# Kernel optimization log

Hardware: AMD Instinct MI355X
Metric: run time of the kernel (lower is better)

The kernel has to match this reference:

```python
import jax, jax.numpy as jnp
import numpy as np

B, S, DIN, H, DOUT, E, SEL = 8, 2048, 512, 512, 512, 262144, 512
N = B * S


def setup_inputs() -> dict:
    key = jax.random.key(0)
    ks = jax.random.split(key, 20)
    inp = {
        "x": jax.random.normal(ks[0], (B, S, DIN), dtype=jnp.float32),
        "edge_index": jax.random.randint(ks[1], (2, E), 0, N, dtype=jnp.int64),
        "selected_idx": jax.random.randint(ks[2], (B, SEL), 0, S, dtype=jnp.int64),
        "edge_label": jax.random.randint(ks[3], (E,), 0, 8, dtype=jnp.int64),
    }
    k = 4
    for l, fin in enumerate([DIN, H, H]):
        inp[f"conv{l}_w1"] = jax.random.normal(ks[k], (2 * fin, H), dtype=jnp.float32) * 0.02; k += 1
        inp[f"conv{l}_b1"] = jnp.full((H,), 0.01, dtype=jnp.float32)
        inp[f"conv{l}_w2"] = jax.random.normal(ks[k], (H, H), dtype=jnp.float32) * 0.02; k += 1
        inp[f"conv{l}_b2"] = jnp.full((H,), 0.01, dtype=jnp.float32)
    inp["ffn_w1"] = jax.random.normal(ks[k], (H, H), dtype=jnp.float32) * 0.02; k += 1
    inp["ffn_b1"] = jnp.full((H,), 0.01, dtype=jnp.float32)
    inp["ffn_w2"] = jax.random.normal(ks[k], (H, DOUT), dtype=jnp.float32) * 0.02; k += 1
    inp["ffn_b2"] = jnp.full((DOUT,), 0.01, dtype=jnp.float32)
    return inp


def _ffw(x, w1, b1, w2, b2):
    # FeedForward: fc2(act_dropout(relu(fc1(x)))), dropout=0 in eval
    return jax.nn.relu(x @ w1 + b1) @ w2 + b2


def reference(x, edge_index, selected_idx, edge_label,
              conv0_w1, conv0_b1, conv0_w2, conv0_b2,
              conv1_w1, conv1_b1, conv1_w2, conv1_b2,
              conv2_w1, conv2_b1, conv2_w2, conv2_b2,
              ffn_w1, ffn_b1, ffn_w2, ffn_b2):
    b, s, d = x.shape
    n = b * s
    h = x.reshape(n, d)
    src, dst = edge_index[0], edge_index[1]  # PyG: x_j = source, x_i = target
    convs = [(conv0_w1, conv0_b1, conv0_w2, conv0_b2),
             (conv1_w1, conv1_b1, conv1_w2, conv1_b2),
             (conv2_w1, conv2_b1, conv2_w2, conv2_b2)]
    for w1, b1, w2, b2 in convs:
        xi = h[dst]                                   # [E, F]
        xj = h[src]
        ef = jnp.concatenate([xi, xj - xi], axis=1)   # [E, 2F]
        m = _ffw(ef, w1, b1, w2, b2)                  # per-edge MLP [E, H]
        agg = jax.ops.segment_max(m, dst, num_segments=n)
        agg = jnp.where(jnp.isneginf(agg), 0.0, agg)  # empty segments -> 0 (PyG fill)
        h = jax.nn.relu(agg)                          # dropout p acts as identity in eval
    h = _ffw(h, ffn_w1, ffn_b1, ffn_w2, ffn_b2)
    out = h.reshape(b, s, -1)                         # [B, S, DOUT]
    idx = jnp.broadcast_to(selected_idx[:, :, None], (b, selected_idx.shape[1], out.shape[-1]))
    return jnp.take_along_axis(out, idx, axis=1)      # [B, SEL, DOUT]
```

## Files before the change

### kernel.cpp

```cpp
#include <hip/hip_runtime.h>
#include <hip/hip_bf16.h>


#define N_NODES 16384
#define EDGES   262144
#define HDIM    512
#define SEQ     2048

typedef __attribute__((ext_vector_type(8))) short short8;
typedef __attribute__((ext_vector_type(8))) _Float16 half8;
typedef __attribute__((ext_vector_type(2))) _Float16 half2v;
typedef __attribute__((ext_vector_type(4))) float f32x4;

__device__ __forceinline__ void gld16(const void* g, void* l) {
    __builtin_amdgcn_global_load_lds(
        (const __attribute__((address_space(1))) void*)g,
        (__attribute__((address_space(3))) void*)l, 16, 0, 0);
}
__device__ __forceinline__ unsigned short f2b(float f) {
    unsigned int x = __float_as_uint(f);
    return (unsigned short)((x + 0x7fffu + ((x >> 16) & 1u)) >> 16);
}
__device__ __forceinline__ unsigned short f2h(float f) {
    _Float16 h = (_Float16)f;
    return __builtin_bit_cast(unsigned short, h);
}
__device__ __forceinline__ unsigned int zpack_h(unsigned int u, unsigned int v) {
    half2v a = __builtin_bit_cast(half2v, u);
    half2v b = __builtin_bit_cast(half2v, v);
    half2v s = a + b;
    half2v z = {(_Float16)0.f, (_Float16)0.f};
    half2v r = __builtin_elementwise_max(s, z);
    return __builtin_bit_cast(unsigned int, r);
}
__device__ __forceinline__ short8 frag_ld(const short* S, int row, int q) {
    int p = q ^ ((row >> 1) & 3);
    return *(const short8*)(S + row * 32 + p * 8);
}
__device__ __forceinline__ void stage_tile(const short* G, int kc, short* S, int t) {
#pragma unroll
    for (int it = 0; it < 2; ++it) {
        int lin = it * 256 + t;
        int row = lin >> 2, p = lin & 3;
        int q = p ^ ((row >> 1) & 3);
        gld16(G + (size_t)row * HDIM + kc + q * 8, S + lin * 8);
    }
}
__device__ __forceinline__ void mfma_tile_bf16(const short* As, const short* Bs,
                                               int wm, int wn, int l, f32x4 acc[4][4]) {
    short8 a[4], b[4];
#pragma unroll
    for (int mt = 0; mt < 4; ++mt) a[mt] = frag_ld(As, wm + mt * 16 + (l & 15), l >> 4);
#pragma unroll
    for (int nt = 0; nt < 4; ++nt) b[nt] = frag_ld(Bs, wn + nt * 16 + (l & 15), l >> 4);
#pragma unroll
    for (int mt = 0; mt < 4; ++mt)
#pragma unroll
        for (int nt = 0; nt < 4; ++nt)
            acc[mt][nt] = __builtin_amdgcn_mfma_f32_16x16x32_bf16(a[mt], b[nt], acc[mt][nt], 0, 0, 0);
}
__device__ __forceinline__ half8 frag64(const short* S, int row, int q) {
    int p = q ^ ((row >> 1) & 7) ^ (row & 1);
    return *(const half8*)(S + row * 64 + p * 8);
}
__device__ __forceinline__ void stageB32(const short* __restrict__ Wt, int n0, int col0,
                                         short* buf, int t) {
#pragma unroll
    for (int it = 0; it < 4; ++it) {
        int lin = it * 256 + t;
        int row = lin >> 2, s = lin & 3;
        int q = s ^ ((row >> 1) & 3);
        gld16(Wt + (size_t)(n0 + row) * HDIM + col0 + q * 8, buf + lin * 8);
    }
}

__global__ __launch_bounds__(256) void hist_kernel(
    const int* __restrict__ dst, int* __restrict__ hist) {
    int idx = blockIdx.x * 256 + threadIdx.x;
    atomicAdd(&hist[dst[idx]], 1);
}
__global__ __launch_bounds__(256) void scan_kernel(
    const int* __restrict__ hist, int* __restrict__ cursor) {
    __shared__ int part[256];
    const int t = threadIdx.x, base = t * 64;
    int sum = 0;
    for (int i = 0; i < 64; ++i) sum += hist[base + i];
    part[t] = sum;
    __syncthreads();
    int run = 0;
    for (int i = 0; i < t; ++i) run += part[i];
    for (int i = 0; i < 64; ++i) {
        int h = hist[base + i];
        cursor[base + i] = run;
        run += h;
    }
}
__global__ __launch_bounds__(256) void scatter_kernel(
    const int* __restrict__ dst, const int* __restrict__ src,
    int* __restrict__ cursor, int* __restrict__ dstS, int* __restrict__ srcS) {
    int idx = blockIdx.x * 256 + threadIdx.x;
    int d = dst[idx];
    int p = atomicAdd(&cursor[d], 1);
    dstS[p] = d;
    srcS[p] = src[idx];
}

__global__ __launch_bounds__(256) void prep_weights_kernel(
    const float* __restrict__ w1, const float* __restrict__ w2,
    short* __restrict__ WdT, short* __restrict__ w1bT, short* __restrict__ W2T) {
    __shared__ float tile[32][33];
    const int which = blockIdx.z;
    const int k0 = blockIdx.x * 32, n0 = blockIdx.y * 32;
    const int tx = threadIdx.x, ty = threadIdx.y;
#pragma unroll
    for (int i = 0; i < 4; ++i) {
        int k = k0 + ty + i * 8, n = n0 + tx;
        float v;
        if (which == 0)      v = w1[k * 512 + n] - w1[(k + 512) * 512 + n];
        else if (which == 1) v = w1[(k + 512) * 512 + n];
        else                 v = w2[k * 512 + n];
        tile[ty + i * 8][tx] = v;
    }
    __syncthreads();
    short* out = which == 0 ? WdT : (which == 1 ? w1bT : W2T);
#pragma unroll
    for (int i = 0; i < 4; ++i) {
        int n = n0 + ty + i * 8, k = k0 + tx;
        float v = tile[tx][ty + i * 8];
        out[(size_t)n * 512 + k] = (short)(which == 2 ? f2h(v) : f2b(v));
    }
}
__global__ __launch_bounds__(256) void tr_kernel(
    const float* __restrict__ W1, const float* __restrict__ W2,
    short* __restrict__ T1, short* __restrict__ T2) {
    __shared__ float tile[32][33];
    const float* W = blockIdx.z ? W2 : W1;
    short* T = blockIdx.z ? T2 : T1;
    const int k0 = blockIdx.x * 32, n0 = blockIdx.y * 32;
    const int tx = threadIdx.x, ty = threadIdx.y;
#pragma unroll
    for (int i = 0; i < 4; ++i)
        tile[ty + i * 8][tx] = W[(k0 + ty + i * 8) * 512 + n0 + tx];
    __syncthreads();
#pragma unroll
    for (int i = 0; i < 4; ++i)
        T[(size_t)(n0 + ty + i * 8) * 512 + k0 + tx] = (short)f2b(tile[tx][ty + i * 8]);
}
__global__ __launch_bounds__(256) void cvt_bf16_kernel(
    const float* __restrict__ x, short* __restrict__ xb) {
    int idx = blockIdx.x * 256 + threadIdx.x;
    float4 v = ((const float4*)x)[idx];
    uint2 o;
    o.x = (unsigned int)f2b(v.x) | ((unsigned int)f2b(v.y) << 16);
    o.y = (unsigned int)f2b(v.z) | ((unsigned int)f2b(v.w) << 16);
    ((uint2*)xb)[idx] = o;
}

__global__ __launch_bounds__(256) void node_gemm_uv_kernel(
    const short* __restrict__ A, const short* __restrict__ WdT,
    const short* __restrict__ w1bT, const float* __restrict__ b1,
    short* __restrict__ U, short* __restrict__ V) {
    __shared__ short As[128 * 32];
    __shared__ short Bs[128 * 32];
    const int t = threadIdx.x;
    const int by = blockIdx.y;
    const short* Wt = (by < 4) ? WdT : w1bT;
    short* C = (by < 4) ? U : V;
    const float* bias = (by < 4) ? b1 : nullptr;
    const int m0 = blockIdx.x * 128, n0 = (by & 3) * 128;
    const int w = t >> 6, l = t & 63;
    const int wm = (w & 1) * 64, wn = (w >> 1) * 64;
    f32x4 acc[4][4] = {};
    for (int kc = 0; kc < HDIM; kc += 32) {
        stage_tile(A + (size_t)m0 * HDIM, kc, As, t);
        stage_tile(Wt + (size_t)n0 * HDIM, kc, Bs, t);
        __syncthreads();
        mfma_tile_bf16(As, Bs, wm, wn, l, acc);
        __syncthreads();
    }
#pragma unroll
    for (int mt = 0; mt < 4; ++mt) {
        int m = m0 + wm + mt * 16 + (l >> 4) * 4;
#pragma unroll
        for (int nt = 0; nt < 4; ++nt) {
            int n = n0 + wn + nt * 16 + (l & 15);
            float bv = bias ? bias[n] : 0.f;
#pragma unroll
            for (int r = 0; r < 4; ++r)
                C[(size_t)(m + r) * HDIM + n] = (short)f2h(acc[mt][nt][r] + bv);
        }
    }
}

__device__ __forceinline__ unsigned int fkey(float m) {
    unsigned int b = __float_as_uint(m);
    return ((int)b < 0) ? ~b : (b | 0x80000000u);
}
__device__ __forceinline__ void kflush(unsigned int* K, int d, int col, float m) {
    atomicMax(K + (((size_t)d) << 9) + col, fkey(m));
}
__global__ __launch_bounds__(256, 3) void edge_mfma_kernel(
    const short* __restrict__ U, const short* __restrict__ V,
    const short* __restrict__ Wt, const int* __restrict__ srcS,
    const int* __restrict__ dstS, unsigned int* __restrict__ K) {
    __shared__ short As[64 * 64];
    __shared__ short Bs[2][256 * 32];
    __shared__ int sdst[64], ssrc[64];
    const int t = threadIdx.x;
    const int L  = blockIdx.x;
    const int g  = (L >> 4) * 8 + (L & 7);
    const int nh = (L >> 3) & 1;
    const int e0 = g * 64, n0 = nh * 256;
    if (t < 64) { sdst[t] = dstS[e0 + t]; ssrc[t] = srcS[e0 + t]; }
    __syncthreads();
    const int w = t >> 6, l = t & 63;
    const int wnb = w * 64;
    const int lm = l & 15;
    const int arow = t >> 2, s0 = (t & 3) * 2;
    const int perm = ((arow >> 1) & 7) ^ (arow & 1);
    const int p0 = s0 ^ perm, p1 = (s0 + 1) ^ perm;
    const short* up = U + (((size_t)sdst[arow]) << 9) + s0 * 8;
    const short* vp = V + (((size_t)ssrc[arow]) << 9) + s0 * 8;
    unsigned int* As_u = (unsigned int*)As;
    f32x4 acc[4][4] = {};
    uint4 pu0, pu1, pv0, pv1, nu0, nu1, nv0, nv1;
    stageB32(Wt, n0, 0, Bs[0], t);
    pu0 = *(const uint4*)(up);
    pu1 = *(const uint4*)(up + 8);
    pv0 = *(const uint4*)(vp);
    pv1 = *(const uint4*)(vp + 8);
#pragma unroll
    for (int hh = 0; hh < 16; ++hh) {
        const int kc = (hh >> 1) * 64;
        if (hh < 15) {
            const int c1 = ((hh + 1) >> 1) * 64 + ((hh + 1) & 1) * 32;
            stageB32(Wt, n0, c1, Bs[(hh + 1) & 1], t);
        }
        if ((hh & 1) == 0) {
            if (hh < 14) {
                nu0 = *(const uint4*)(up + kc + 64);
                nu1 = *(const uint4*)(up + kc + 64 + 8);
                nv0 = *(const uint4*)(vp + kc + 64);
                nv1 = *(const uint4*)(vp + kc + 64 + 8);
            }
            uint4 z0, z1;
            z0.x = zpack_h(pu0.x, pv0.x); z0.y = zpack_h(pu0.y, pv0.y);
            z0.z = zpack_h(pu0.z, pv0.z); z0.w = zpack_h(pu0.w, pv0.w);
            z1.x = zpack_h(pu1.x, pv1.x); z1.y = zpack_h(pu1.y, pv1.y);
            z1.z = zpack_h(pu1.z, pv1.z); z1.w = zpack_h(pu1.w, pv1.w);
            *(uint4*)(As_u + arow * 32 + p0 * 4) = z0;
            *(uint4*)(As_u + arow * 32 + p1 * 4) = z1;
        }
        if (hh < 14)       asm volatile("s_waitcnt vmcnt(8) lgkmcnt(0)" ::: "memory");
        else if (hh == 14) asm volatile("s_waitcnt vmcnt(4) lgkmcnt(0)" ::: "memory");
        else               asm volatile("s_waitcnt vmcnt(0) lgkmcnt(0)" ::: "memory");
        __builtin_amdgcn_s_barrier();
        asm volatile("" ::: "memory");
        const short* Bb = Bs[hh & 1];
        const int hq = (hh & 1) * 4 + (l >> 4);
        __builtin_amdgcn_s_setprio(1);
        half8 b[4];
#pragma unroll
        for (int nt = 0; nt < 4; ++nt) {
            int row = wnb + nt * 16 + lm;
            int p = (l >> 4) ^ ((row >> 1) & 3);
            b[nt] = *(const half8*)(Bb + row * 32 + p * 8);
        }
#pragma unroll
        for (int mt = 0; mt < 4; ++mt) {
            half8 a = frag64(As, mt * 16 + lm, hq);
#pragma unroll
            for (int nt = 0; nt < 4; ++nt)
                acc[mt][nt] = __builtin_amdgcn_mfma_f32_16x16x32_f16(a, b[nt], acc[mt][nt], 0, 0, 0);
        }
        __builtin_amdgcn_s_setprio(0);
        if ((hh & 1) == 0 && hh < 14) { pu0 = nu0; pu1 = nu1; pv0 = nv0; pv1 = nv1; }
        asm volatile("" ::: "memory");
        __builtin_amdgcn_s_barrier();
    }
    const int dbase = sdst[0];
    const int drange = sdst[63] - dbase + 1;
    unsigned int* tile = (unsigned int*)Bs[1];
    if (drange <= 16) {
#pragma unroll
        for (int i = 0; i < 16; ++i) tile[i * 256 + t] = 0u;
        __syncthreads();
#pragma unroll
        for (int mt = 0; mt < 4; ++mt) {
            int base = mt * 16 + (l >> 4) * 4;
            int d0 = sdst[base], d1 = sdst[base + 1], d2 = sdst[base + 2], d3 = sdst[base + 3];
            int r0 = d0 - dbase, r1 = d1 - dbase, r2 = d2 - dbase, r3 = d3 - dbase;
#pragma unroll
            for (int nt = 0; nt < 4; ++nt) {
                int colb = wnb + nt * 16 + lm;
                f32x4 a = acc[mt][nt];
                float m = a[0];
                if (d1 == d0) m = fmaxf(m, a[1]);
                else { atomicMax(tile + r0 * 256 + colb, fkey(m)); m = a[1]; }
                if (d2 == d1) m = fmaxf(m, a[2]);
                else { atomicMax(tile + r1 * 256 + colb, fkey(m)); m = a[2]; }
                if (d3 == d2) m = fmaxf(m, a[3]);
                else { atomicMax(tile + r2 * 256 + colb, fkey(m)); m = a[3]; }
                atomicMax(tile + r3 * 256 + colb, fkey(m));
            }
        }
        __syncthreads();
#pragma unroll 4
        for (int r = 0; r < 16; ++r) {
            if (r < drange) {
                unsigned int kv = tile[r * 256 + t];
                if (kv) atomicMax(K + (((size_t)(dbase + r)) << 9) + n0 + t, kv);
            }
        }
    } else {
#pragma unroll
        for (int mt = 0; mt < 4; ++mt) {
            int base = mt * 16 + (l >> 4) * 4;
            int d0 = sdst[base], d1 = sdst[base + 1], d2 = sdst[base + 2], d3 = sdst[base + 3];
#pragma unroll
            for (int nt = 0; nt < 4; ++nt) {
                int col = n0 + wnb + nt * 16 + lm;
                f32x4 a = acc[mt][nt];
                float m = a[0];
                if (d1 == d0) m = fmaxf(m, a[1]); else { kflush(K, d0, col, m); m = a[1]; }
                if (d2 == d1) m = fmaxf(m, a[2]); else { kflush(K, d1, col, m); m = a[2]; }
                if (d3 == d2) m = fmaxf(m, a[3]); else { kflush(K, d2, col, m); m = a[3]; }
                kflush(K, d3, col, m);
            }
        }
    }
}

__global__ __launch_bounds__(256) void decode_kernel(
    unsigned int* __restrict__ K, const float* __restrict__ b2,
    short* __restrict__ hb) {
    int idx = blockIdx.x * 256 + threadIdx.x;
    unsigned int k = K[idx];
    K[idx] = 0u;
    int c = idx & (HDIM - 1);
    float v = 0.f;
    if (k != 0u) {
        unsigned int b = (k & 0x80000000u) ? (k ^ 0x80000000u) : ~k;
        v = __uint_as_float(b) + b2[c];
    }
    hb[idx] = (short)f2b(fmaxf(v, 0.f));
}

__global__ __launch_bounds__(256) void gather_bf16_kernel(
    const short* __restrict__ hb, const int* __restrict__ sel,
    short* __restrict__ hgb) {
    int idx = blockIdx.x * 256 + threadIdx.x;
    int row = idx >> 6, c = idx & 63;
    int b = row >> 9;
    int s = sel[row];
    ((uint4*)hgb)[idx] = ((const uint4*)(hb + (((size_t)(b * SEQ + s)) << 9)))[c];
}

__global__ __launch_bounds__(256) void ffn_gemm_kernel(
    const short* __restrict__ A, const short* __restrict__ Wt,
    const float* __restrict__ bias, short* __restrict__ Cb,
    float* __restrict__ Cf, int relu) {
    __shared__ short As[128 * 32];
    __shared__ short Bs[128 * 32];
    const int t = threadIdx.x;
    const int m0 = blockIdx.x * 128, n0 = blockIdx.y * 128;
    const int w = t >> 6, l = t & 63;
    const int wm = (w & 1) * 64, wn = (w >> 1) * 64;
    f32x4 acc[4][4] = {};
    for (int kc = 0; kc < HDIM; kc += 32) {
        stage_tile(A + (size_t)m0 * HDIM, kc, As, t);
        stage_tile(Wt + (size_t)n0 * HDIM, kc, Bs, t);
        __syncthreads();
        mfma_tile_bf16(As, Bs, wm, wn, l, acc);
        __syncthreads();
    }
#pragma unroll
    for (int mt = 0; mt < 4; ++mt) {
        int m = m0 + wm + mt * 16 + (l >> 4) * 4;
#pragma unroll
        for (int nt = 0; nt < 4; ++nt) {
            int n = n0 + wn + nt * 16 + (l & 15);
            float bv = bias[n];
#pragma unroll
            for (int r = 0; r < 4; ++r) {
                float v = acc[mt][nt][r] + bv;
                if (relu) v = fmaxf(v, 0.f);
                if (Cf) Cf[(size_t)(m + r) * HDIM + n] = v;
                else    Cb[(size_t)(m + r) * HDIM + n] = (short)f2b(v);
            }
        }
    }
}

extern "C" void kernel_launch(void* const* d_in, const int* in_sizes, int n_in,
                              void* d_out, int out_size, void* d_ws, size_t ws_size,
                              hipStream_t stream) {
    const float* x   = (const float*)d_in[0];
    const int*   ei  = (const int*)d_in[1];
    const int*   sel = (const int*)d_in[2];
    const int*   src = ei;
    const int*   dst = ei + EDGES;
    const float* cw1[3] = {(const float*)d_in[4],  (const float*)d_in[8],  (const float*)d_in[12]};
    const float* cb1[3] = {(const float*)d_in[5],  (const float*)d_in[9],  (const float*)d_in[13]};
    const float* cw2[3] = {(const float*)d_in[6],  (const float*)d_in[10], (const float*)d_in[14]};
    const float* cb2[3] = {(const float*)d_in[7],  (const float*)d_in[11], (const float*)d_in[15]};
    const float* fw1 = (const float*)d_in[16];
    const float* fb1 = (const float*)d_in[17];
    const float* fw2 = (const float*)d_in[18];
    const float* fb2 = (const float*)d_in[19];
    float* out = (float*)d_out;

    const size_t MB = 1024 * 1024;
    char* p = (char*)d_ws;
    unsigned int* keys = (unsigned int*)p;
    short* U    = (short*)(p + 32 * MB);
    short* V    = (short*)(p + 48 * MB);
    short* hb   = (short*)(p + 64 * MB);
    short* WdT  = (short*)(p + 80 * MB);
    short* w1bT = WdT + 512 * 512;
    short* W2T  = w1bT + 512 * 512;
    short* fw1T = W2T + 512 * 512;
    short* fw2T = fw1T + 512 * 512;
    int*   dstS = (int*)(p + 83 * MB);
    int*   srcS = (int*)(p + 84 * MB);
    int*   hist = (int*)(p + 85 * MB);
    int*   curs = hist + N_NODES;
    short* hgb  = (short*)(p + 86 * MB);
    short* t1b  = (short*)(p + 90 * MB);

    (void)hipMemsetAsync(hist, 0, N_NODES * sizeof(int), stream);
    hist_kernel<<<EDGES / 256, 256, 0, stream>>>(dst, hist);
    scan_kernel<<<1, 256, 0, stream>>>(hist, curs);
    scatter_kernel<<<EDGES / 256, 256, 0, stream>>>(dst, src, curs, dstS, srcS);

    cvt_bf16_kernel<<<8192, 256, 0, stream>>>(x, hb);
    tr_kernel<<<dim3(16, 16, 2), dim3(32, 8), 0, stream>>>(fw1, fw2, fw1T, fw2T);
    (void)hipMemsetAsync(keys, 0, 32 * MB, stream);

    for (int l = 0; l < 3; ++l) {
        prep_weights_kernel<<<dim3(16, 16, 3), dim3(32, 8), 0, stream>>>(
            cw1[l], cw2[l], WdT, w1bT, W2T);
        node_gemm_uv_kernel<<<dim3(128, 8), 256, 0, stream>>>(hb, WdT, w1bT, cb1[l], U, V);
        edge_mfma_kernel<<<8192, 256, 0, stream>>>(U, V, W2T, srcS, dstS, keys);
        decode_kernel<<<(N_NODES * HDIM) / 256, 256, 0, stream>>>(keys, cb2[l], hb);
    }

    gather_bf16_kernel<<<(4096 * 64) / 256, 256, 0, stream>>>(hb, sel, hgb);
    ffn_gemm_kernel<<<dim3(32, 4), 256, 0, stream>>>(hgb, fw1T, fb1, t1b, nullptr, 1);
    ffn_gemm_kernel<<<dim3(32, 4), 256, 0, stream>>>(t1b, fw2T, fb2, nullptr, out, 0);
}
```

Baseline: 870.1 us.

## Raise edge kernel occupancy, drop shared index staging, store interior rows directly

Raises the launch-bounds occupancy hint from 3 to 4 waves per SIMD. Edge indices are now read directly from global memory instead of being staged through shared memory behind a barrier. The separate next-chunk prefetch registers are removed by reloading into the current registers right after they are written to LDS. The tile is zeroed with vector stores. In the flush, rows strictly inside the block's sorted destination range get a plain store instead of an atomicMax, relying on other blocks never touching those rows. That assumption only holds if edges are sorted by destination and a segment never spans two blocks, so the plain-store path risks wrong results otherwise. The main intent is to cut register pressure, barriers and atomic traffic.

After: 879.7 us. Within noise of the previous version (+1.1%).

```diff
diff --git a/kernel.cpp b/kernel.cpp
--- a/kernel.cpp
+++ b/kernel.cpp
@@ -199,31 +199,30 @@
 __device__ __forceinline__ void kflush(unsigned int* K, int d, int col, float m) {
     atomicMax(K + (((size_t)d) << 9) + col, fkey(m));
 }
-__global__ __launch_bounds__(256, 3) void edge_mfma_kernel(
+__global__ __launch_bounds__(256, 4) void edge_mfma_kernel(
     const short* __restrict__ U, const short* __restrict__ V,
     const short* __restrict__ Wt, const int* __restrict__ srcS,
     const int* __restrict__ dstS, unsigned int* __restrict__ K) {
     __shared__ short As[64 * 64];
     __shared__ short Bs[2][256 * 32];
-    __shared__ int sdst[64], ssrc[64];
     const int t = threadIdx.x;
     const int L  = blockIdx.x;
     const int g  = (L >> 4) * 8 + (L & 7);
     const int nh = (L >> 3) & 1;
     const int e0 = g * 64, n0 = nh * 256;
-    if (t < 64) { sdst[t] = dstS[e0 + t]; ssrc[t] = srcS[e0 + t]; }
-    __syncthreads();
     const int w = t >> 6, l = t & 63;
     const int wnb = w * 64;
     const int lm = l & 15;
     const int arow = t >> 2, s0 = (t & 3) * 2;
     const int perm = ((arow >> 1) & 7) ^ (arow & 1);
     const int p0 = s0 ^ perm, p1 = (s0 + 1) ^ perm;
-    const short* up = U + (((size_t)sdst[arow]) << 9) + s0 * 8;
-    const short* vp = V + (((size_t)ssrc[arow]) << 9) + s0 * 8;
+    const int drow = dstS[e0 + arow];
+    const int srow = srcS[e0 + arow];
+    const short* up = U + (((size_t)drow) << 9) + s0 * 8;
+    const short* vp = V + (((size_t)srow) << 9) + s0 * 8;
     unsigned int* As_u = (unsigned int*)As;
     f32x4 acc[4][4] = {};
-    uint4 pu0, pu1, pv0, pv1, nu0, nu1, nv0, nv1;
+    uint4 pu0, pu1, pv0, pv1;
     stageB32(Wt, n0, 0, Bs[0], t);
     pu0 = *(const uint4*)(up);
     pu1 = *(const uint4*)(up + 8);
@@ -237,12 +236,6 @@
             stageB32(Wt, n0, c1, Bs[(hh + 1) & 1], t);
         }
         if ((hh & 1) == 0) {
-            if (hh < 14) {
-                nu0 = *(const uint4*)(up + kc + 64);
-                nu1 = *(const uint4*)(up + kc + 64 + 8);
-                nv0 = *(const uint4*)(vp + kc + 64);
-                nv1 = *(const uint4*)(vp + kc + 64 + 8);
-            }
             uint4 z0, z1;
             z0.x = zpack_h(pu0.x, pv0.x); z0.y = zpack_h(pu0.y, pv0.y);
             z0.z = zpack_h(pu0.z, pv0.z); z0.w = zpack_h(pu0.w, pv0.w);
@@ -250,6 +243,12 @@
             z1.z = zpack_h(pu1.z, pv1.z); z1.w = zpack_h(pu1.w, pv1.w);
             *(uint4*)(As_u + arow * 32 + p0 * 4) = z0;
             *(uint4*)(As_u + arow * 32 + p1 * 4) = z1;
+            if (hh < 14) {
+                pu0 = *(const uint4*)(up + kc + 64);
+                pu1 = *(const uint4*)(up + kc + 64 + 8);
+                pv0 = *(const uint4*)(vp + kc + 64);
+                pv1 = *(const uint4*)(vp + kc + 64 + 8);
+            }
         }
         if (hh < 14)       asm volatile("s_waitcnt vmcnt(8) lgkmcnt(0)" ::: "memory");
         else if (hh == 14) asm volatile("s_waitcnt vmcnt(4) lgkmcnt(0)" ::: "memory");
@@ -274,32 +273,32 @@
                 acc[mt][nt] = __builtin_amdgcn_mfma_f32_16x16x32_f16(a, b[nt], acc[mt][nt], 0, 0, 0);
         }
         __builtin_amdgcn_s_setprio(0);
-        if ((hh & 1) == 0 && hh < 14) { pu0 = nu0; pu1 = nu1; pv0 = nv0; pv1 = nv1; }
         asm volatile("" ::: "memory");
         __builtin_amdgcn_s_barrier();
     }
-    const int dbase = sdst[0];
-    const int drange = sdst[63] - dbase + 1;
+    const int dbase = dstS[e0];
+    const int drange = dstS[e0 + 63] - dbase + 1;
     unsigned int* tile = (unsigned int*)Bs[1];
     if (drange <= 16) {
-#pragma unroll
-        for (int i = 0; i < 16; ++i) tile[i * 256 + t] = 0u;
+        uint4 zz = {0u, 0u, 0u, 0u};
+#pragma unroll
+        for (int i = 0; i < 4; ++i) ((uint4*)tile)[i * 256 + t] = zz;
         __syncthreads();
 #pragma unroll
         for (int mt = 0; mt < 4; ++mt) {
             int base = mt * 16 + (l >> 4) * 4;
-            int d0 = sdst[base], d1 = sdst[base + 1], d2 = sdst[base + 2], d3 = sdst[base + 3];
-            int r0 = d0 - dbase, r1 = d1 - dbase, r2 = d2 - dbase, r3 = d3 - dbase;
+            const int4 dd = *(const int4*)(dstS + e0 + base);
+            int r0 = dd.x - dbase, r1 = dd.y - dbase, r2 = dd.z - dbase, r3 = dd.w - dbase;
 #pragma unroll
             for (int nt = 0; nt < 4; ++nt) {
                 int colb = wnb + nt * 16 + lm;
                 f32x4 a = acc[mt][nt];
                 float m = a[0];
-                if (d1 == d0) m = fmaxf(m, a[1]);
+                if (r1 == r0) m = fmaxf(m, a[1]);
                 else { atomicMax(tile + r0 * 256 + colb, fkey(m)); m = a[1]; }
-                if (d2 == d1) m = fmaxf(m, a[2]);
+                if (r2 == r1) m = fmaxf(m, a[2]);
                 else { atomicMax(tile + r1 * 256 + colb, fkey(m)); m = a[2]; }
-                if (d3 == d2) m = fmaxf(m, a[3]);
+                if (r3 == r2) m = fmaxf(m, a[3]);
                 else { atomicMax(tile + r2 * 256 + colb, fkey(m)); m = a[3]; }
                 atomicMax(tile + r3 * 256 + colb, fkey(m));
             }
@@ -309,14 +308,19 @@
         for (int r = 0; r < 16; ++r) {
             if (r < drange) {
                 unsigned int kv = tile[r * 256 + t];
-                if (kv) atomicMax(K + (((size_t)(dbase + r)) << 9) + n0 + t, kv);
+                if (kv) {
+                    unsigned int* addr = K + (((size_t)(dbase + r)) << 9) + n0 + t;
+                    if (r > 0 && r < drange - 1) *addr = kv;
+                    else atomicMax(addr, kv);
+                }
             }
         }
     } else {
 #pragma unroll
         for (int mt = 0; mt < 4; ++mt) {
             int base = mt * 16 + (l >> 4) * 4;
-            int d0 = sdst[base], d1 = sdst[base + 1], d2 = sdst[base + 2], d3 = sdst[base + 3];
+            const int4 dd = *(const int4*)(dstS + e0 + base);
+            int d0 = dd.x, d1 = dd.y, d2 = dd.z, d3 = dd.w;
 #pragma unroll
             for (int nt = 0; nt < 4; ++nt) {
                 int col = n0 + wnb + nt * 16 + lm;
```
